# Performance work log

Hardware: AMD Instinct MI355X
Metric: run time of the kernel (lower is better)

The kernel has to match this reference:

```python
import jax, jax.numpy as jnp
import numpy as np


def setup_inputs() -> dict:
    key = jax.random.key(0)
    k1, k2, k3, k4, k5 = jax.random.split(key, 5)
    B, Q, M, P, C = 32, 256, 128, 64, 20
    return {
        "pred_logits": jax.random.normal(k1, (B, Q, C + 1), dtype=jnp.float32),
        "pred_polylines": jax.random.normal(k2, (B, Q, P, 2), dtype=jnp.float32),
        "target_polylines": jax.random.normal(k3, (B, M, P, 2), dtype=jnp.float32),
        "src_idx": jax.random.randint(k4, (B, M), 0, Q),
        "labels": jax.random.randint(k5, (B, M), 0, C),
    }


def reference(pred_logits, pred_polylines, target_polylines, src_idx, labels):
    B, Q, C1 = pred_logits.shape
    num_classes = C1 - 1
    M = src_idx.shape[1]
    num_polylines = jnp.maximum(jnp.float32(B * M), 1.0)
    batch_ix = jnp.arange(B)[:, None]  # [B,1]

    # ---- classification loss (cross entropy, unmatched queries -> no-object class) ----
    target_classes = jnp.full((B, Q), num_classes, dtype=jnp.int32)
    target_classes = target_classes.at[batch_ix, src_idx].set(labels.astype(jnp.int32))
    logp = jax.nn.log_softmax(pred_logits, axis=-1)  # [B,Q,C+1]
    loss_ce = -jnp.take_along_axis(logp, target_classes[..., None], axis=-1).mean()

    # ---- polyline loss: symmetric chamfer-style mean of min L1 distances ----
    src_poly = pred_polylines[batch_ix, src_idx]  # [B,M,P,2]
    # all-pairs L1 distance matrix per matched pair: [B,M,P,P]
    dist = jnp.abs(src_poly[:, :, :, None, :] - target_polylines[:, :, None, :, :]).sum(-1)
    min1 = dist.min(axis=2).mean(axis=-1)  # min over src points, mean over tgt points: [B,M]
    min2 = dist.min(axis=3).mean(axis=-1)  # min over tgt points, mean over src points: [B,M]
    loss_polyline = ((min1 + min2) * 0.5).sum() / num_polylines

    # ---- direction loss: 1 - cosine(start->end vectors) ----
    eps = 1e-6
    sd = src_poly[:, :, -1] - src_poly[:, :, 0]  # [B,M,2]
    td = target_polylines[:, :, -1] - target_polylines[:, :, 0]
    sd = sd / (jnp.linalg.norm(sd, axis=-1, keepdims=True) + eps)
    td = td / (jnp.linalg.norm(td, axis=-1, keepdims=True) + eps)
    cos = (sd * td).sum(-1)  # [B,M]
    loss_direction = (1.0 - cos).sum() / num_polylines

    return jnp.stack([loss_ce, loss_polyline, loss_direction])
```

## Files before the change

### kernel.cpp

```cpp
#include <hip/hip_runtime.h>
#include <math.h>

constexpr int kB = 32;
constexpr int kQ = 256;
constexpr int kM = 128;
constexpr int kP = 64;
constexpr int kC = 20;
constexpr int kC1 = kC + 1;

constexpr int kPairsPerBlock = 16;
constexpr int kBlocks = (kB * kM) / kPairsPerBlock;

constexpr int kWsPoly = 0;
constexpr int kWsDir  = 1024;
constexpr int kWsCe   = 2048;
constexpr int kWsCnt  = 2304;

__global__ __launch_bounds__(256) void fused_kernel(const float* __restrict__ logits,
                                                    const float2* __restrict__ pred_poly,
                                                    const float2* __restrict__ tgt_poly,
                                                    const int* __restrict__ src_idx,
                                                    const int* __restrict__ labels,
                                                    float* __restrict__ ws,
                                                    float* __restrict__ out) {
    const int tid  = threadIdx.x;
    const int lane = tid & 63;
    const int w    = tid >> 6;
    const int bid  = blockIdx.x;

    __shared__ float2 s_src[kPairsPerBlock][kP];
    __shared__ float2 s_tgt[kPairsPerBlock][kP];
    __shared__ int    s_sidx[kPairsPerBlock];
    __shared__ int    c_idx[kM];
    __shared__ int    c_lab[kM];
    __shared__ int    s_last;
    __shared__ float  sp[4], sd[4], sc[4];

    const int base = bid * kPairsPerBlock;
    const int b    = base >> 7;

    if (tid < kPairsPerBlock) s_sidx[tid] = src_idx[base + tid];
    if (tid < kM) {
        c_idx[tid] = src_idx[b * kM + tid];
        c_lab[tid] = labels[b * kM + tid];
    }
    __syncthreads();

    #pragma unroll
    for (int i = 0; i < 4; ++i) {
        const int g      = i * 256 + tid;
        const int p      = g >> 6;
        const int within = g & 63;
        if (within < 32) {
            const float4* s4 = reinterpret_cast<const float4*>(
                pred_poly + (size_t)(b * kQ + s_sidx[p]) * kP);
            reinterpret_cast<float4*>(s_src[p])[within] = s4[within];
        } else {
            const float4* t4 = reinterpret_cast<const float4*>(
                tgt_poly + (size_t)(base + p) * kP);
            reinterpret_cast<float4*>(s_tgt[p])[within - 32] = t4[within - 32];
        }
    }
    __syncthreads();

    float accPoly = 0.f, accDir = 0.f;
    #pragma unroll
    for (int i = 0; i < 4; ++i) {
        const int p = w * 4 + i;
        const float2 ms = s_src[p][lane];
        const float2 mt = s_tgt[p][lane];
        const float4* srow = reinterpret_cast<const float4*>(s_src[p]);
        const float4* trow = reinterpret_cast<const float4*>(s_tgt[p]);
        float minJ = 1e30f, minI = 1e30f;
        #pragma unroll 8
        for (int jj = 0; jj < kP / 2; ++jj) {
            const float4 tj = trow[jj];
            const float4 sj = srow[jj];
            minJ = fminf(minJ, fminf(fabsf(ms.x - tj.x) + fabsf(ms.y - tj.y),
                                     fabsf(ms.x - tj.z) + fabsf(ms.y - tj.w)));
            minI = fminf(minI, fminf(fabsf(sj.x - mt.x) + fabsf(sj.y - mt.y),
                                     fabsf(sj.z - mt.x) + fabsf(sj.w - mt.y)));
        }
        float val = minI + minJ;
        #pragma unroll
        for (int off = 32; off > 0; off >>= 1) val += __shfl_down(val, off, 64);
        if (lane == 0) {
            accPoly += val;
            const float2 s0 = s_src[p][0], s1 = s_src[p][kP - 1];
            const float2 t0 = s_tgt[p][0], t1 = s_tgt[p][kP - 1];
            const float sdx = s1.x - s0.x, sdy = s1.y - s0.y;
            const float tdx = t1.x - t0.x, tdy = t1.y - t0.y;
            const float sn = sqrtf(sdx * sdx + sdy * sdy) + 1e-6f;
            const float tn = sqrtf(tdx * tdx + tdy * tdy) + 1e-6f;
            accDir += 1.0f - (sdx * tdx + sdy * tdy) / (sn * tn);
        }
    }
    if (lane == 0) {
        const int wid = bid * 4 + w;
        __hip_atomic_store(&ws[kWsPoly + wid], accPoly, __ATOMIC_RELAXED, __HIP_MEMORY_SCOPE_AGENT);
        __hip_atomic_store(&ws[kWsDir + wid],  accDir,  __ATOMIC_RELAXED, __HIP_MEMORY_SCOPE_AGENT);
    }

    if (w == 0) {
        float ceVal = 0.f;
        if (lane < 32) {
            const int q = ((bid & 7) << 5) + lane;
            int tc = kC;
            #pragma unroll 4
            for (int m = 0; m < kM; ++m) {
                if (c_idx[m] == q) tc = c_lab[m];
            }
            const float* lp = logits + (size_t)(b * kQ + q) * kC1;
            float mx = -1e30f;
            #pragma unroll
            for (int c = 0; c < kC1; ++c) mx = fmaxf(mx, lp[c]);
            float se = 0.f, vt = 0.f;
            #pragma unroll
            for (int c = 0; c < kC1; ++c) {
                const float x = lp[c];
                se += __expf(x - mx);
                if (c == tc) vt = x;
            }
            ceVal = -(vt - mx - __logf(se));
        }
        #pragma unroll
        for (int off = 32; off > 0; off >>= 1) ceVal += __shfl_down(ceVal, off, 64);
        if (lane == 0)
            __hip_atomic_store(&ws[kWsCe + bid], ceVal, __ATOMIC_RELAXED, __HIP_MEMORY_SCOPE_AGENT);
    }

    __syncthreads();
    if (tid == 0) {
        unsigned int* cnt = reinterpret_cast<unsigned int*>(ws + kWsCnt);
        const unsigned int old =
            __hip_atomic_fetch_add(cnt, 1u, __ATOMIC_ACQ_REL, __HIP_MEMORY_SCOPE_AGENT);
        s_last = (old == (unsigned int)(kBlocks - 1));
    }
    __syncthreads();
    if (!s_last) return;

    float p = 0.f, d = 0.f, c = 0.f;
    #pragma unroll
    for (int k = 0; k < 4; ++k) {
        p += __hip_atomic_load(&ws[kWsPoly + tid + 256 * k], __ATOMIC_RELAXED, __HIP_MEMORY_SCOPE_AGENT);
        d += __hip_atomic_load(&ws[kWsDir  + tid + 256 * k], __ATOMIC_RELAXED, __HIP_MEMORY_SCOPE_AGENT);
    }
    c = __hip_atomic_load(&ws[kWsCe + tid], __ATOMIC_RELAXED, __HIP_MEMORY_SCOPE_AGENT);

    #pragma unroll
    for (int off = 32; off > 0; off >>= 1) {
        p += __shfl_down(p, off, 64);
        d += __shfl_down(d, off, 64);
        c += __shfl_down(c, off, 64);
    }

    if (lane == 0) { sp[w] = p; sd[w] = d; sc[w] = c; }
    __syncthreads();
    if (tid == 0) {
        const float P = sp[0] + sp[1] + sp[2] + sp[3];
        const float D = sd[0] + sd[1] + sd[2] + sd[3];
        const float C = sc[0] + sc[1] + sc[2] + sc[3];
        out[0] = C * (1.0f / (float)(kB * kQ));
        out[1] = P * (0.5f / ((float)kP * (float)(kB * kM)));
        out[2] = D * (1.0f / (float)(kB * kM));
    }
}

extern "C" void kernel_launch(void* const* d_in, const int* in_sizes, int n_in,
                              void* d_out, int out_size, void* d_ws, size_t ws_size,
                              hipStream_t stream) {
    const float*  pred_logits = (const float*)d_in[0];
    const float2* pred_poly   = (const float2*)d_in[1];
    const float2* tgt_poly    = (const float2*)d_in[2];
    const int*    src_idx     = (const int*)d_in[3];
    const int*    labels      = (const int*)d_in[4];
    float* out = (float*)d_out;
    float* ws  = (float*)d_ws;

    hipMemsetAsync(ws + kWsCnt, 0, sizeof(unsigned int), stream);

    fused_kernel<<<kBlocks, 256, 0, stream>>>(
        pred_logits, pred_poly, tgt_poly, src_idx, labels, ws, out);
}
```

Baseline: 84.20 us.

## Replace last-block atomic counter reduction with separate finalize kernel

Drops the memset plus atomic-counter last-block pattern. A second single-block kernel now does the final reduction, and each block pre-reduces its per-wave poly and direction sums in shared memory, so it writes one value per block instead of four. This removes the memset launch and the acq_rel atomic per block, at the cost of an extra kernel launch and an inter-kernel dependency.

```diff
diff --git a/kernel.cpp b/kernel.cpp
--- a/kernel.cpp
+++ b/kernel.cpp
@@ -12,17 +12,15 @@
 constexpr int kBlocks = (kB * kM) / kPairsPerBlock;
 
 constexpr int kWsPoly = 0;
-constexpr int kWsDir  = 1024;
-constexpr int kWsCe   = 2048;
-constexpr int kWsCnt  = 2304;
+constexpr int kWsDir  = 256;
+constexpr int kWsCe   = 512;
 
-__global__ __launch_bounds__(256) void fused_kernel(const float* __restrict__ logits,
-                                                    const float2* __restrict__ pred_poly,
-                                                    const float2* __restrict__ tgt_poly,
-                                                    const int* __restrict__ src_idx,
-                                                    const int* __restrict__ labels,
-                                                    float* __restrict__ ws,
-                                                    float* __restrict__ out) {
+__global__ __launch_bounds__(256) void partial_kernel(const float* __restrict__ logits,
+                                                      const float2* __restrict__ pred_poly,
+                                                      const float2* __restrict__ tgt_poly,
+                                                      const int* __restrict__ src_idx,
+                                                      const int* __restrict__ labels,
+                                                      float* __restrict__ ws) {
     const int tid  = threadIdx.x;
     const int lane = tid & 63;
     const int w    = tid >> 6;
@@ -33,8 +31,7 @@
     __shared__ int    s_sidx[kPairsPerBlock];
     __shared__ int    c_idx[kM];
     __shared__ int    c_lab[kM];
-    __shared__ int    s_last;
-    __shared__ float  sp[4], sd[4], sc[4];
+    __shared__ float  sp[4], sd[4];
 
     const int base = bid * kPairsPerBlock;
     const int b    = base >> 7;
@@ -95,11 +92,6 @@
             accDir += 1.0f - (sdx * tdx + sdy * tdy) / (sn * tn);
         }
     }
-    if (lane == 0) {
-        const int wid = bid * 4 + w;
-        __hip_atomic_store(&ws[kWsPoly + wid], accPoly, __ATOMIC_RELAXED, __HIP_MEMORY_SCOPE_AGENT);
-        __hip_atomic_store(&ws[kWsDir + wid],  accDir,  __ATOMIC_RELAXED, __HIP_MEMORY_SCOPE_AGENT);
-    }
 
     if (w == 0) {
         float ceVal = 0.f;
@@ -125,27 +117,26 @@
         }
         #pragma unroll
         for (int off = 32; off > 0; off >>= 1) ceVal += __shfl_down(ceVal, off, 64);
-        if (lane == 0)
-            __hip_atomic_store(&ws[kWsCe + bid], ceVal, __ATOMIC_RELAXED, __HIP_MEMORY_SCOPE_AGENT);
+        if (lane == 0) ws[kWsCe + bid] = ceVal;
     }
 
+    if (lane == 0) { sp[w] = accPoly; sd[w] = accDir; }
     __syncthreads();
     if (tid == 0) {
-        unsigned int* cnt = reinterpret_cast<unsigned int*>(ws + kWsCnt);
-        const unsigned int old =
-            __hip_atomic_fetch_add(cnt, 1u, __ATOMIC_ACQ_REL, __HIP_MEMORY_SCOPE_AGENT);
-        s_last = (old == (unsigned int)(kBlocks - 1));
+        ws[kWsPoly + bid] = sp[0] + sp[1] + sp[2] + sp[3];
+        ws[kWsDir + bid]  = sd[0] + sd[1] + sd[2] + sd[3];
     }
-    __syncthreads();
-    if (!s_last) return;
+}
 
-    float p = 0.f, d = 0.f, c = 0.f;
-    #pragma unroll
-    for (int k = 0; k < 4; ++k) {
-        p += __hip_atomic_load(&ws[kWsPoly + tid + 256 * k], __ATOMIC_RELAXED, __HIP_MEMORY_SCOPE_AGENT);
-        d += __hip_atomic_load(&ws[kWsDir  + tid + 256 * k], __ATOMIC_RELAXED, __HIP_MEMORY_SCOPE_AGENT);
-    }
-    c = __hip_atomic_load(&ws[kWsCe + tid], __ATOMIC_RELAXED, __HIP_MEMORY_SCOPE_AGENT);
+__global__ __launch_bounds__(256) void finalize_kernel(const float* __restrict__ ws,
+                                                       float* __restrict__ out) {
+    const int tid  = threadIdx.x;
+    const int lane = tid & 63;
+    const int w    = tid >> 6;
+
+    float p = ws[kWsPoly + tid];
+    float d = ws[kWsDir + tid];
+    float c = ws[kWsCe + tid];
 
     #pragma unroll
     for (int off = 32; off > 0; off >>= 1) {
@@ -154,6 +145,7 @@
         c += __shfl_down(c, off, 64);
     }
 
+    __shared__ float sp[4], sd[4], sc[4];
     if (lane == 0) { sp[w] = p; sd[w] = d; sc[w] = c; }
     __syncthreads();
     if (tid == 0) {
@@ -177,8 +169,7 @@
     float* out = (float*)d_out;
     float* ws  = (float*)d_ws;
 
-    hipMemsetAsync(ws + kWsCnt, 0, sizeof(unsigned int), stream);
-
-    fused_kernel<<<kBlocks, 256, 0, stream>>>(
-        pred_logits, pred_poly, tgt_poly, src_idx, labels, ws, out);
+    partial_kernel<<<kBlocks, 256, 0, stream>>>(
+        pred_logits, pred_poly, tgt_poly, src_idx, labels, ws);
+    finalize_kernel<<<1, 256, 0, stream>>>(ws, out);
 }
```

Result: faster. 78.18 us (-7.1%).
